# Performance work log

Hardware: AMD Instinct MI355X
Metric: run time of the kernel (lower is better)

Reference implementation:

```python
import jax, jax.numpy as jnp
import numpy as np

ATT = 512  # attention_size

def setup_inputs() -> dict:
    key = jax.random.key(0)
    k0, k1, k2, k3, k4 = jax.random.split(key, 5)
    B, Sq, Sk, Din, Dmem = 32, 1024, 1024, 512, 512
    inputs = jax.random.normal(k0, (B, Sq, Din), dtype=jnp.float32)
    memory = jax.random.normal(k1, (B, Sk, Dmem), dtype=jnp.float32)
    memory_mask = jax.random.randint(k2, (B, Sk), 0, 2).astype(jnp.int32)
    W_input = (jax.random.normal(k3, (Din, ATT), dtype=jnp.float32) * 0.02)
    W_memory = (jax.random.normal(k4, (Dmem, ATT), dtype=jnp.float32) * 0.02)
    return {"inputs": inputs, "memory": memory, "memory_mask": memory_mask,
            "W_input": W_input, "W_memory": W_memory}

def reference(inputs, memory, memory_mask, W_input, W_memory):
    # projections (bias=False) + ReLU; dropout=0 -> identity
    x = jax.nn.relu(jnp.einsum('bqd,da->bqa', inputs, W_input))   # [B,Sq,A]
    m = jax.nn.relu(jnp.einsum('bkd,da->bka', memory, W_memory))  # [B,Sk,A]
    scale = 1.0 / jnp.sqrt(jnp.asarray(ATT, dtype=inputs.dtype))
    logits = jnp.einsum('bqa,bka->bqk', x, m) * scale             # [B,Sq,Sk]
    mask = (memory_mask[:, None, :] != 0)                         # [B,1,Sk] broadcast over Sq
    logits = jnp.where(mask, logits, jnp.asarray(-1e30, dtype=logits.dtype))
    score = jax.nn.softmax(logits, axis=-1)
    context = jnp.einsum('bqk,bkd->bqd', score, memory)           # [B,Sq,Dmem]
    return jnp.concatenate([context, inputs], axis=-1)            # [B,Sq,Dmem+Din]
```

## Files before the change

kernel.cpp:

```cpp
#include <hip/hip_runtime.h>

typedef __bf16 bf16x8 __attribute__((ext_vector_type(8)));
typedef float f32x4 __attribute__((ext_vector_type(4)));

__device__ __forceinline__ unsigned short f2bf(float f) {
    union { float f; unsigned u; } v; v.f = f;
    unsigned r = v.u + 0x7FFFu + ((v.u >> 16) & 1u);
    return (unsigned short)(r >> 16);
}

__global__ __launch_bounds__(256) void prep_kernel(
    const float4* __restrict__ inputs4, uint2* __restrict__ InB16,
    float4* __restrict__ out4,
    const float* __restrict__ W0, const float* __restrict__ W1,
    unsigned short* __restrict__ D0, unsigned short* __restrict__ D1,
    const int* __restrict__ mask,
    int* __restrict__ cnt, int* __restrict__ padded,
    float4* __restrict__ rowsum4,
    const float* __restrict__ memory,
    unsigned short* __restrict__ MemG, unsigned short* __restrict__ MemGT)
{
    __shared__ float tile[32][33];
    __shared__ float tileG[32][132];
    __shared__ int wsum[4];
    __shared__ int kidx32[32];
    const int bid = blockIdx.x;
    const int t = threadIdx.x;

    if (bid < 1024) {
        const int b = bid >> 5;
        const int jt = bid & 31;
        const int j0 = jt * 32;
        const int* m = mask + b * 1024;
        int v[4]; int s = 0;
#pragma unroll
        for (int e = 0; e < 4; e++) { v[e] = (m[t * 4 + e] != 0) ? 1 : 0; s += v[e]; }
        const int lane = t & 63, wv = t >> 6;
        int x = s;
#pragma unroll
        for (int off = 1; off < 64; off <<= 1) {
            int y = __shfl_up(x, off, 64);
            if (lane >= off) x += y;
        }
        if (lane == 63) wsum[wv] = x;
        __syncthreads();
        int base = 0;
        for (int w = 0; w < wv; w++) base += wsum[w];
        const int nb = wsum[0] + wsum[1] + wsum[2] + wsum[3];
        const int pb = (nb + 127) & ~127;
        if (j0 >= pb) return;
        int pos = base + x - s;
#pragma unroll
        for (int e = 0; e < 4; e++)
            if (v[e]) {
                int p = pos++;
                if (p >= j0 && p < j0 + 32) kidx32[p - j0] = t * 4 + e;
            }
        __syncthreads();

        const float4* src4 = (const float4*)(memory + (size_t)b * 1024 * 512);
        const int jj = t >> 3;
        const int cq = t & 7;
        const bool live = (j0 + jj) < nb;
        const int krow = live ? kidx32[jj] : 0;

        float4 vv[4][4];
        if (live) {
            const float4* rp = src4 + (size_t)krow * 128 + cq * 4;
#pragma unroll
            for (int c = 0; c < 4; c++)
#pragma unroll
                for (int i = 0; i < 4; i++) vv[c][i] = rp[c * 32 + i];
        } else {
#pragma unroll
            for (int c = 0; c < 4; c++)
#pragma unroll
                for (int i = 0; i < 4; i++) vv[c][i] = float4{0.f, 0.f, 0.f, 0.f};
        }

        unsigned short* mg = MemG + (size_t)b * 1024 * 512 + (size_t)(j0 + jj) * 512;
#pragma unroll
        for (int c = 0; c < 4; c++) {
            union { unsigned short u[16]; uint4 q[2]; } pk;
#pragma unroll
            for (int i = 0; i < 4; i++) {
                pk.u[i * 4 + 0] = f2bf(vv[c][i].x); pk.u[i * 4 + 1] = f2bf(vv[c][i].y);
                pk.u[i * 4 + 2] = f2bf(vv[c][i].z); pk.u[i * 4 + 3] = f2bf(vv[c][i].w);
            }
            *(uint4*)&mg[c * 128 + cq * 16] = pk.q[0];
            *(uint4*)&mg[c * 128 + cq * 16 + 8] = pk.q[1];
        }

        const int dd = t >> 1;
        const int jh = (t & 1) * 16;
        unsigned short* gtb = MemGT + (size_t)b * 512 * 1024 + j0 + jh;
#pragma unroll
        for (int c = 0; c < 4; c++) {
#pragma unroll
            for (int i = 0; i < 4; i++)
                *(float4*)&tileG[jj][cq * 16 + i * 4] = vv[c][i];
            __syncthreads();
            union { unsigned short u[16]; uint4 q[2]; } pt;
#pragma unroll
            for (int k = 0; k < 16; k++) pt.u[k] = f2bf(tileG[jh + k][dd]);
            unsigned short* gt = gtb + (size_t)(c * 128 + dd) * 1024;
            *(uint4*)&gt[0] = pt.q[0];
            *(uint4*)&gt[8] = pt.q[1];
            __syncthreads();
        }
    } else if (bid < 1056) {
        const int b = bid - 1024;
        rowsum4[b * 256 + t] = float4{0.f, 0.f, 0.f, 0.f};
        const int* m = mask + b * 1024;
        int s = 0;
#pragma unroll
        for (int e = 0; e < 4; e++) s += (m[t * 4 + e] != 0) ? 1 : 0;
        const int lane = t & 63, wv = t >> 6;
        int x = s;
#pragma unroll
        for (int off = 1; off < 64; off <<= 1) {
            int y = __shfl_up(x, off, 64);
            if (lane >= off) x += y;
        }
        if (lane == 63) wsum[wv] = x;
        __syncthreads();
        if (t == 255) {
            int total = wsum[0] + wsum[1] + wsum[2] + wsum[3];
            cnt[b] = total;
            padded[b] = (total + 127) & ~127;
        }
    } else if (bid < 1568) {
        const int tb = bid - 1056;
        const float* src = (tb >> 8) ? W1 : W0;
        unsigned short* dst = (tb >> 8) ? D1 : D0;
        const int rem = tb & 255;
        const int s0 = (rem & 15) * 32, d0 = (rem >> 4) * 32;
        const int tr = t >> 5, tc = t & 31;
#pragma unroll
        for (int i = 0; i < 4; i++)
            tile[tr + i * 8][tc] = src[(size_t)(s0 + tr + i * 8) * 512 + d0 + tc];
        __syncthreads();
#pragma unroll
        for (int i = 0; i < 4; i++)
            dst[(size_t)(d0 + tr + i * 8) * 512 + s0 + tc] = f2bf(tile[tc][tr + i * 8]);
    } else {
        const int i = (bid - 1568) * 256 + t;
        const int bq = i >> 7;
        const int d  = i & 127;
        float4 v = inputs4[i];
        out4[(size_t)bq * 256 + 128 + d] = v;
        union { unsigned short u[4]; uint2 p; } pk;
        pk.u[0] = f2bf(v.x); pk.u[1] = f2bf(v.y);
        pk.u[2] = f2bf(v.z); pk.u[3] = f2bf(v.w);
        InB16[i] = pk.p;
    }
}

template<int CMODE>
__device__ __forceinline__ void gemm_core(
    unsigned char* lds,
    const unsigned short* __restrict__ Ab, const unsigned short* __restrict__ Bb,
    void* __restrict__ Cb, float* __restrict__ rs, int nbv,
    int rowA, int rowB, int Kz, int lda, int ldb, int ldc, float scale)
{
    const int nt = Kz >> 6;

    const int t = threadIdx.x;
    const int w = t >> 6;
    const int lane = t & 63;
    const int wm = w >> 2;
    const int wn = w & 3;
    const int l15 = lane & 15;
    const int sx = (((lane >> 4) ^ ((l15 >> 1) & 3)) << 4);

    const int r0 = t >> 2;
    const int sl = (t & 3) ^ ((t >> 3) & 3);
    const unsigned short* aS0 = Ab + (size_t)(rowA + r0) * lda + sl * 8;
    const unsigned short* aS1 = aS0 + (size_t)128 * lda;
    const unsigned short* bS0 = Bb + (size_t)(rowB + r0) * ldb + sl * 8;
    const unsigned short* bS1 = bS0 + (size_t)128 * ldb;

    const int wofs = w * 1024;
    const int aRd = (wm * 128 + l15) * 64 + sx;
    const int bRd = 32768 + (wn * 64 + l15) * 64 + sx;

    f32x4 acc[8][4];
#pragma unroll
    for (int i = 0; i < 8; i++)
#pragma unroll
        for (int j = 0; j < 4; j++) acc[i][j] = f32x4{0.f, 0.f, 0.f, 0.f};

#define GLL(SRC, DOFS) __builtin_amdgcn_global_load_lds(                        \
        (const __attribute__((address_space(1))) void*)(SRC),                   \
        (__attribute__((address_space(3))) void*)&lds[DOFS], 16, 0, 0)
#define STAGEA(BUF, KH, KEL) do {                                               \
        GLL(aS0 + (KEL), (BUF) * 65536 + (KH) * 16384 + wofs);                  \
        GLL(aS1 + (KEL), (BUF) * 65536 + (KH) * 16384 + wofs + 8192); } while (0)
#define STAGEB(BUF, KH, KEL) do {                                               \
        GLL(bS0 + (KEL), (BUF) * 65536 + 32768 + (KH) * 16384 + wofs);          \
        GLL(bS1 + (KEL), (BUF) * 65536 + 32768 + (KH) * 16384 + wofs + 8192); } while (0)

    STAGEA(0, 0, 0); STAGEB(0, 0, 0); STAGEA(0, 1, 32); STAGEB(0, 1, 32);
    asm volatile("s_waitcnt vmcnt(4)" ::: "memory");
    __builtin_amdgcn_s_barrier();

    for (int tt = 0; tt < nt; ++tt) {
        const int cur = (tt & 1) * 65536;
        const int nxt = (tt & 1) ^ 1;
        const bool pf = (tt + 1) < nt;
        const int kn = (tt + 1) * 64;
        bf16x8 af[4], bf0[4], bf1[4];

#pragma unroll
        for (int i = 0; i < 4; i++) af[i]  = *(const bf16x8*)&lds[cur + aRd + i * 1024];
#pragma unroll
        for (int j = 0; j < 4; j++) bf0[j] = *(const bf16x8*)&lds[cur + bRd + j * 1024];
        if (pf) STAGEA(nxt, 0, kn);
        __builtin_amdgcn_s_barrier();
        asm volatile("s_waitcnt lgkmcnt(0)" ::: "memory");
        __builtin_amdgcn_sched_barrier(0);
        __builtin_amdgcn_s_setprio(1);
#pragma unroll
        for (int i = 0; i < 4; i++)
#pragma unroll
            for (int j = 0; j < 4; j++)
                acc[i][j] = __builtin_amdgcn_mfma_f32_16x16x32_bf16(af[i], bf0[j], acc[i][j], 0, 0, 0);
        __builtin_amdgcn_s_setprio(0);
        __builtin_amdgcn_s_barrier();

#pragma unroll
        for (int i = 0; i < 4; i++) af[i] = *(const bf16x8*)&lds[cur + aRd + (i + 4) * 1024];
        if (pf) STAGEB(nxt, 0, kn);
        __builtin_amdgcn_s_barrier();
        asm volatile("s_waitcnt lgkmcnt(0)" ::: "memory");
        __builtin_amdgcn_sched_barrier(0);
        __builtin_amdgcn_s_setprio(1);
#pragma unroll
        for (int i = 0; i < 4; i++)
#pragma unroll
            for (int j = 0; j < 4; j++)
                acc[i + 4][j] = __builtin_amdgcn_mfma_f32_16x16x32_bf16(af[i], bf0[j], acc[i + 4][j], 0, 0, 0);
        __builtin_amdgcn_s_setprio(0);
        if (pf) { asm volatile("s_waitcnt vmcnt(4)" ::: "memory"); }
        else    { asm volatile("s_waitcnt vmcnt(0)" ::: "memory"); }
        __builtin_amdgcn_s_barrier();

#pragma unroll
        for (int i = 0; i < 4; i++) af[i]  = *(const bf16x8*)&lds[cur + 16384 + aRd + i * 1024];
#pragma unroll
        for (int j = 0; j < 4; j++) bf1[j] = *(const bf16x8*)&lds[cur + 16384 + bRd + j * 1024];
        if (pf) STAGEA(nxt, 1, kn + 32);
        __builtin_amdgcn_s_barrier();
        asm volatile("s_waitcnt lgkmcnt(0)" ::: "memory");
        __builtin_amdgcn_sched_barrier(0);
        __builtin_amdgcn_s_setprio(1);
#pragma unroll
        for (int i = 0; i < 4; i++)
#pragma unroll
            for (int j = 0; j < 4; j++)
                acc[i][j] = __builtin_amdgcn_mfma_f32_16x16x32_bf16(af[i], bf1[j], acc[i][j], 0, 0, 0);
        __builtin_amdgcn_s_setprio(0);
        __builtin_amdgcn_s_barrier();

#pragma unroll
        for (int i = 0; i < 4; i++) af[i] = *(const bf16x8*)&lds[cur + 16384 + aRd + (i + 4) * 1024];
        if (pf) STAGEB(nxt, 1, kn + 32);
        __builtin_amdgcn_s_barrier();
        asm volatile("s_waitcnt lgkmcnt(0)" ::: "memory");
        __builtin_amdgcn_sched_barrier(0);
        __builtin_amdgcn_s_setprio(1);
#pragma unroll
        for (int i = 0; i < 4; i++)
#pragma unroll
            for (int j = 0; j < 4; j++)
                acc[i + 4][j] = __builtin_amdgcn_mfma_f32_16x16x32_bf16(af[i], bf1[j], acc[i + 4][j], 0, 0, 0);
        __builtin_amdgcn_s_setprio(0);
        if (pf) { asm volatile("s_waitcnt vmcnt(4)" ::: "memory"); }
        __builtin_amdgcn_s_barrier();
    }

#undef GLL
#undef STAGEA
#undef STAGEB

    const int orow = (lane >> 4) * 4;
    const int ocol = l15;

    if constexpr (CMODE == 0) {
        unsigned short* C = (unsigned short*)Cb;
#pragma unroll
        for (int mf = 0; mf < 8; mf++)
#pragma unroll
            for (int nf = 0; nf < 4; nf++) {
                const int col = rowB + wn * 64 + nf * 16 + ocol;
#pragma unroll
                for (int r = 0; r < 4; r++) {
                    const int rw = rowA + wm * 128 + mf * 16 + orow + r;
                    C[(size_t)rw * ldc + col] = f2bf(fmaxf(acc[mf][nf][r], 0.f));
                }
            }
    } else if constexpr (CMODE == 1) {
        unsigned short* C = (unsigned short*)Cb;
#pragma unroll
        for (int mf = 0; mf < 8; mf++) {
            float part[4] = {0.f, 0.f, 0.f, 0.f};
#pragma unroll
            for (int nf = 0; nf < 4; nf++) {
                const int col = rowB + wn * 64 + nf * 16 + ocol;
#pragma unroll
                for (int r = 0; r < 4; r++) {
                    float p = (col < nbv) ? __expf(acc[mf][nf][r] * scale) : 0.f;
                    part[r] += p;
                    const int rw = rowA + wm * 128 + mf * 16 + orow + r;
                    C[(size_t)rw * ldc + col] = f2bf(p);
                }
            }
#pragma unroll
            for (int r = 0; r < 4; r++) {
                float s = part[r];
                s += __shfl_xor(s, 1, 64);
                s += __shfl_xor(s, 2, 64);
                s += __shfl_xor(s, 4, 64);
                s += __shfl_xor(s, 8, 64);
                if (ocol == 0)
                    atomicAdd(&rs[rowA + wm * 128 + mf * 16 + orow + r], s);
            }
        }
    } else {
        float* C = (float*)Cb;
#pragma unroll
        for (int mf = 0; mf < 8; mf++) {
            float inv[4];
#pragma unroll
            for (int r = 0; r < 4; r++)
                inv[r] = 1.0f / rs[rowA + wm * 128 + mf * 16 + orow + r];
#pragma unroll
            for (int nf = 0; nf < 4; nf++) {
                const int col = rowB + wn * 64 + nf * 16 + ocol;
#pragma unroll
                for (int r = 0; r < 4; r++) {
                    const int rw = rowA + wm * 128 + mf * 16 + orow + r;
                    C[(size_t)rw * ldc + col] = acc[mf][nf][r] * inv[r];
                }
            }
        }
    }
}

__global__ __launch_bounds__(512, 2) void gemm_proj_kernel(
    const unsigned short* __restrict__ InB16, const unsigned short* __restrict__ WtIn,
    unsigned short* __restrict__ Xq,
    const unsigned short* __restrict__ MemG, const unsigned short* __restrict__ WtMem,
    unsigned short* __restrict__ Xm, const int* __restrict__ padded)
{
    __shared__ __align__(16) unsigned char lds[131072];
    const int id = blockIdx.x;
    const int xcd = id & 7, slot = id >> 3;
    const int y = xcd + 8 * (slot >> 1);
    const int x = slot & 1;
    const int rowB = x * 256;
    const unsigned short* A;
    const unsigned short* Bt;
    unsigned short* C;
    int rowA;
    if (y < 128) {
        A = InB16; Bt = WtIn; C = Xq; rowA = y * 256;
    } else {
        const int idx = y - 128;
        const int z = idx >> 2;
        rowA = (idx & 3) * 256;
        if (rowA >= padded[z]) return;
        A = MemG + (size_t)z * 524288;
        Bt = WtMem;
        C = Xm + (size_t)z * 524288;
    }
    gemm_core<0>(lds, A, Bt, (void*)C, nullptr, 0, rowA, rowB,
                 512, 512, 512, 512, 0.f);
}

__global__ __launch_bounds__(512, 2) void gemm_p_kernel(
    const unsigned short* __restrict__ Xq, const unsigned short* __restrict__ Xm,
    unsigned short* __restrict__ P, const int* __restrict__ cnt,
    const int* __restrict__ padded, float* __restrict__ rowsum, float scale)
{
    __shared__ __align__(16) unsigned char lds[131072];
    const int id = blockIdx.x;
    const int xcd = id & 7, slot = id >> 3;
    const int z = xcd + 8 * (slot >> 4);
    const int r = slot & 15;
    const int x = r & 3, y = r >> 2;
    const int rowB = x * 256;
    if (rowB >= padded[z]) return;
    gemm_core<1>(lds, Xq + (size_t)z * 524288, Xm + (size_t)z * 524288,
                 (void*)(P + (size_t)z * 1048576), rowsum + (size_t)z * 1024, cnt[z],
                 y * 256, rowB, 512, 512, 512, 1024, scale);
}

__global__ __launch_bounds__(512, 2) void gemm_ctx_kernel(
    const unsigned short* __restrict__ P, const unsigned short* __restrict__ MemGT,
    float* __restrict__ out, const int* __restrict__ padded, float* __restrict__ rowsum)
{
    __shared__ __align__(16) unsigned char lds[131072];
    const int id = blockIdx.x;
    const int xcd = id & 7, slot = id >> 3;
    const int z = xcd + 8 * (slot >> 3);
    const int r = slot & 7;
    const int x = r & 1, y = r >> 1;
    gemm_core<2>(lds, P + (size_t)z * 1048576, MemGT + (size_t)z * 524288,
                 (void*)(out + (size_t)z * 1048576), rowsum + (size_t)z * 1024, 0,
                 y * 256, x * 256, padded[z],
                 1024, 1024, 1024, 1.f);
}

extern "C" void kernel_launch(void* const* d_in, const int* in_sizes, int n_in,
                              void* d_out, int out_size, void* d_ws, size_t ws_size,
                              hipStream_t stream)
{
    const float* inputs = (const float*)d_in[0];
    const float* memory = (const float*)d_in[1];
    const int*   mmask  = (const int*)d_in[2];
    const float* W_in   = (const float*)d_in[3];
    const float* W_mem  = (const float*)d_in[4];
    float* out = (float*)d_out;

    char* ws = (char*)d_ws;
    const unsigned long long MB = 1048576ull;
    unsigned short* Wt_in  = (unsigned short*)(ws);
    unsigned short* Wt_mem = (unsigned short*)(ws + 524288);
    unsigned short* InB16  = (unsigned short*)(ws + 1 * MB);
    unsigned short* MemG   = (unsigned short*)(ws + 33 * MB);
    unsigned short* P      = (unsigned short*)(ws + 1 * MB);
    unsigned short* MemGT  = (unsigned short*)(ws + 65 * MB);
    unsigned short* Xq     = (unsigned short*)(ws + 97 * MB);
    unsigned short* Xm     = (unsigned short*)(ws + 129 * MB);
    float*          rowsum = (float*)(ws + 161 * MB);
    int*            cntp   = (int*)(ws + 161 * MB + 262144);
    int*            padp   = (int*)(ws + 161 * MB + 262144 + 128);

    const float scale = 0.04419417382415922f;

    prep_kernel<<<17952, 256, 0, stream>>>(
        (const float4*)inputs, (uint2*)InB16, (float4*)out,
        W_in, W_mem, Wt_in, Wt_mem,
        mmask, cntp, padp, (float4*)rowsum,
        memory, MemG, MemGT);

    gemm_proj_kernel<<<512, 512, 0, stream>>>(
        InB16, Wt_in, Xq, MemG, Wt_mem, Xm, padp);

    gemm_p_kernel<<<512, 512, 0, stream>>>(
        Xq, Xm, P, cntp, padp, rowsum, scale);

    gemm_ctx_kernel<<<256, 512, 0, stream>>>(
        P, MemGT, out, padp, rowsum);
}
```

Before: 363.4 us.

## Shrink GEMM block tiles to 128x128 with 4 waves and more blocks

Changes the shared GEMM core from 256x256 tiles with 8 waves to 128x128 tiles with 4 waves, each wave computing a 64x64 sub-tile. LDS is halved to 64 KB, the k-loop is restructured into two half-steps, and all three GEMM kernels are relaunched with four times as many 256-thread blocks using new XCD-aware index mappings. The aim is better load balance and occupancy, especially where padding-based early exits leave 256-wide tiles idle. In exchange, each block reuses less data, so global and LDS traffic per FLOP goes up.

Result: no change. 366.8 us (+0.9%).

```diff
diff --git a/kernel.cpp b/kernel.cpp
--- a/kernel.cpp
+++ b/kernel.cpp
@@ -168,25 +168,25 @@
     const int t = threadIdx.x;
     const int w = t >> 6;
     const int lane = t & 63;
-    const int wm = w >> 2;
-    const int wn = w & 3;
+    const int wm = w >> 1;
+    const int wn = w & 1;
     const int l15 = lane & 15;
     const int sx = (((lane >> 4) ^ ((l15 >> 1) & 3)) << 4);
 
     const int r0 = t >> 2;
     const int sl = (t & 3) ^ ((t >> 3) & 3);
     const unsigned short* aS0 = Ab + (size_t)(rowA + r0) * lda + sl * 8;
-    const unsigned short* aS1 = aS0 + (size_t)128 * lda;
+    const unsigned short* aS1 = aS0 + (size_t)64 * lda;
     const unsigned short* bS0 = Bb + (size_t)(rowB + r0) * ldb + sl * 8;
-    const unsigned short* bS1 = bS0 + (size_t)128 * ldb;
+    const unsigned short* bS1 = bS0 + (size_t)64 * ldb;
 
     const int wofs = w * 1024;
-    const int aRd = (wm * 128 + l15) * 64 + sx;
-    const int bRd = 32768 + (wn * 64 + l15) * 64 + sx;
-
-    f32x4 acc[8][4];
-#pragma unroll
-    for (int i = 0; i < 8; i++)
+    const int aRd = (wm * 64 + l15) * 64 + sx;
+    const int bRd = 16384 + (wn * 64 + l15) * 64 + sx;
+
+    f32x4 acc[4][4];
+#pragma unroll
+    for (int i = 0; i < 4; i++)
 #pragma unroll
         for (int j = 0; j < 4; j++) acc[i][j] = f32x4{0.f, 0.f, 0.f, 0.f};
 
@@ -194,28 +194,28 @@
         (const __attribute__((address_space(1))) void*)(SRC),                   \
         (__attribute__((address_space(3))) void*)&lds[DOFS], 16, 0, 0)
 #define STAGEA(BUF, KH, KEL) do {                                               \
-        GLL(aS0 + (KEL), (BUF) * 65536 + (KH) * 16384 + wofs);                  \
-        GLL(aS1 + (KEL), (BUF) * 65536 + (KH) * 16384 + wofs + 8192); } while (0)
+        GLL(aS0 + (KEL), (BUF) * 32768 + (KH) * 8192 + wofs);                   \
+        GLL(aS1 + (KEL), (BUF) * 32768 + (KH) * 8192 + wofs + 4096); } while (0)
 #define STAGEB(BUF, KH, KEL) do {                                               \
-        GLL(bS0 + (KEL), (BUF) * 65536 + 32768 + (KH) * 16384 + wofs);          \
-        GLL(bS1 + (KEL), (BUF) * 65536 + 32768 + (KH) * 16384 + wofs + 8192); } while (0)
+        GLL(bS0 + (KEL), (BUF) * 32768 + 16384 + (KH) * 8192 + wofs);           \
+        GLL(bS1 + (KEL), (BUF) * 32768 + 16384 + (KH) * 8192 + wofs + 4096); } while (0)
 
     STAGEA(0, 0, 0); STAGEB(0, 0, 0); STAGEA(0, 1, 32); STAGEB(0, 1, 32);
     asm volatile("s_waitcnt vmcnt(4)" ::: "memory");
     __builtin_amdgcn_s_barrier();
 
     for (int tt = 0; tt < nt; ++tt) {
-        const int cur = (tt & 1) * 65536;
+        const int cur = (tt & 1) * 32768;
         const int nxt = (tt & 1) ^ 1;
         const bool pf = (tt + 1) < nt;
         const int kn = (tt + 1) * 64;
-        bf16x8 af[4], bf0[4], bf1[4];
+        bf16x8 af[4], bfr[4];
 
 #pragma unroll
         for (int i = 0; i < 4; i++) af[i]  = *(const bf16x8*)&lds[cur + aRd + i * 1024];
 #pragma unroll
-        for (int j = 0; j < 4; j++) bf0[j] = *(const bf16x8*)&lds[cur + bRd + j * 1024];
-        if (pf) STAGEA(nxt, 0, kn);
+        for (int j = 0; j < 4; j++) bfr[j] = *(const bf16x8*)&lds[cur + bRd + j * 1024];
+        if (pf) { STAGEA(nxt, 0, kn); STAGEB(nxt, 0, kn); }
         __builtin_amdgcn_s_barrier();
         asm volatile("s_waitcnt lgkmcnt(0)" ::: "memory");
         __builtin_amdgcn_sched_barrier(0);
@@ -224,13 +224,17 @@
         for (int i = 0; i < 4; i++)
 #pragma unroll
             for (int j = 0; j < 4; j++)
-                acc[i][j] = __builtin_amdgcn_mfma_f32_16x16x32_bf16(af[i], bf0[j], acc[i][j], 0, 0, 0);
+                acc[i][j] = __builtin_amdgcn_mfma_f32_16x16x32_bf16(af[i], bfr[j], acc[i][j], 0, 0, 0);
         __builtin_amdgcn_s_setprio(0);
+        if (pf) { asm volatile("s_waitcnt vmcnt(4)" ::: "memory"); }
+        else    { asm volatile("s_waitcnt vmcnt(0)" ::: "memory"); }
         __builtin_amdgcn_s_barrier();
 
 #pragma unroll
-        for (int i = 0; i < 4; i++) af[i] = *(const bf16x8*)&lds[cur + aRd + (i + 4) * 1024];
-        if (pf) STAGEB(nxt, 0, kn);
+        for (int i = 0; i < 4; i++) af[i]  = *(const bf16x8*)&lds[cur + 8192 + aRd + i * 1024];
+#pragma unroll
+        for (int j = 0; j < 4; j++) bfr[j] = *(const bf16x8*)&lds[cur + 8192 + bRd + j * 1024];
+        if (pf) { STAGEA(nxt, 1, kn + 32); STAGEB(nxt, 1, kn + 32); }
         __builtin_amdgcn_s_barrier();
         asm volatile("s_waitcnt lgkmcnt(0)" ::: "memory");
         __builtin_amdgcn_sched_barrier(0);
@@ -239,41 +243,7 @@
         for (int i = 0; i < 4; i++)
 #pragma unroll
             for (int j = 0; j < 4; j++)
-                acc[i + 4][j] = __builtin_amdgcn_mfma_f32_16x16x32_bf16(af[i], bf0[j], acc[i + 4][j], 0, 0, 0);
-        __builtin_amdgcn_s_setprio(0);
-        if (pf) { asm volatile("s_waitcnt vmcnt(4)" ::: "memory"); }
-        else    { asm volatile("s_waitcnt vmcnt(0)" ::: "memory"); }
-        __builtin_amdgcn_s_barrier();
-
-#pragma unroll
-        for (int i = 0; i < 4; i++) af[i]  = *(const bf16x8*)&lds[cur + 16384 + aRd + i * 1024];
-#pragma unroll
-        for (int j = 0; j < 4; j++) bf1[j] = *(const bf16x8*)&lds[cur + 16384 + bRd + j * 1024];
-        if (pf) STAGEA(nxt, 1, kn + 32);
-        __builtin_amdgcn_s_barrier();
-        asm volatile("s_waitcnt lgkmcnt(0)" ::: "memory");
-        __builtin_amdgcn_sched_barrier(0);
-        __builtin_amdgcn_s_setprio(1);
-#pragma unroll
-        for (int i = 0; i < 4; i++)
-#pragma unroll
-            for (int j = 0; j < 4; j++)
-                acc[i][j] = __builtin_amdgcn_mfma_f32_16x16x32_bf16(af[i], bf1[j], acc[i][j], 0, 0, 0);
-        __builtin_amdgcn_s_setprio(0);
-        __builtin_amdgcn_s_barrier();
-
-#pragma unroll
-        for (int i = 0; i < 4; i++) af[i] = *(const bf16x8*)&lds[cur + 16384 + aRd + (i + 4) * 1024];
-        if (pf) STAGEB(nxt, 1, kn + 32);
-        __builtin_amdgcn_s_barrier();
-        asm volatile("s_waitcnt lgkmcnt(0)" ::: "memory");
-        __builtin_amdgcn_sched_barrier(0);
-        __builtin_amdgcn_s_setprio(1);
-#pragma unroll
-        for (int i = 0; i < 4; i++)
-#pragma unroll
-            for (int j = 0; j < 4; j++)
-                acc[i + 4][j] = __builtin_amdgcn_mfma_f32_16x16x32_bf16(af[i], bf1[j], acc[i + 4][j], 0, 0, 0);
+                acc[i][j] = __builtin_amdgcn_mfma_f32_16x16x32_bf16(af[i], bfr[j], acc[i][j], 0, 0, 0);
         __builtin_amdgcn_s_setprio(0);
         if (pf) { asm volatile("s_waitcnt vmcnt(4)" ::: "memory"); }
         __builtin_amdgcn_s_barrier();
@@ -289,20 +259,20 @@
     if constexpr (CMODE == 0) {
         unsigned short* C = (unsigned short*)Cb;
 #pragma unroll
-        for (int mf = 0; mf < 8; mf++)
+        for (int mf = 0; mf < 4; mf++)
 #pragma unroll
             for (int nf = 0; nf < 4; nf++) {
                 const int col = rowB + wn * 64 + nf * 16 + ocol;
 #pragma unroll
                 for (int r = 0; r < 4; r++) {
-                    const int rw = rowA + wm * 128 + mf * 16 + orow + r;
+                    const int rw = rowA + wm * 64 + mf * 16 + orow + r;
                     C[(size_t)rw * ldc + col] = f2bf(fmaxf(acc[mf][nf][r], 0.f));
                 }
             }
     } else if constexpr (CMODE == 1) {
         unsigned short* C = (unsigned short*)Cb;
 #pragma unroll
-        for (int mf = 0; mf < 8; mf++) {
+        for (int mf = 0; mf < 4; mf++) {
             float part[4] = {0.f, 0.f, 0.f, 0.f};
 #pragma unroll
             for (int nf = 0; nf < 4; nf++) {
@@ -311,7 +281,7 @@
                 for (int r = 0; r < 4; r++) {
                     float p = (col < nbv) ? __expf(acc[mf][nf][r] * scale) : 0.f;
                     part[r] += p;
-                    const int rw = rowA + wm * 128 + mf * 16 + orow + r;
+                    const int rw = rowA + wm * 64 + mf * 16 + orow + r;
                     C[(size_t)rw * ldc + col] = f2bf(p);
                 }
             }
@@ -323,23 +293,23 @@
                 s += __shfl_xor(s, 4, 64);
                 s += __shfl_xor(s, 8, 64);
                 if (ocol == 0)
-                    atomicAdd(&rs[rowA + wm * 128 + mf * 16 + orow + r], s);
+                    atomicAdd(&rs[rowA + wm * 64 + mf * 16 + orow + r], s);
             }
         }
     } else {
         float* C = (float*)Cb;
 #pragma unroll
-        for (int mf = 0; mf < 8; mf++) {
+        for (int mf = 0; mf < 4; mf++) {
             float inv[4];
 #pragma unroll
             for (int r = 0; r < 4; r++)
-                inv[r] = 1.0f / rs[rowA + wm * 128 + mf * 16 + orow + r];
+                inv[r] = 1.0f / rs[rowA + wm * 64 + mf * 16 + orow + r];
 #pragma unroll
             for (int nf = 0; nf < 4; nf++) {
                 const int col = rowB + wn * 64 + nf * 16 + ocol;
 #pragma unroll
                 for (int r = 0; r < 4; r++) {
-                    const int rw = rowA + wm * 128 + mf * 16 + orow + r;
+                    const int rw = rowA + wm * 64 + mf * 16 + orow + r;
                     C[(size_t)rw * ldc + col] = acc[mf][nf][r] * inv[r];
                 }
             }
@@ -347,28 +317,28 @@
     }
 }
 
-__global__ __launch_bounds__(512, 2) void gemm_proj_kernel(
+__global__ __launch_bounds__(256, 2) void gemm_proj_kernel(
     const unsigned short* __restrict__ InB16, const unsigned short* __restrict__ WtIn,
     unsigned short* __restrict__ Xq,
     const unsigned short* __restrict__ MemG, const unsigned short* __restrict__ WtMem,
     unsigned short* __restrict__ Xm, const int* __restrict__ padded)
 {
-    __shared__ __align__(16) unsigned char lds[131072];
+    __shared__ __align__(16) unsigned char lds[65536];
     const int id = blockIdx.x;
-    const int xcd = id & 7, slot = id >> 3;
-    const int y = xcd + 8 * (slot >> 1);
-    const int x = slot & 1;
-    const int rowB = x * 256;
+    const int xcd = id & 7, u8 = id >> 3;
+    const int y = xcd + 8 * (u8 >> 2);
+    const int x = u8 & 3;
+    const int rowB = x * 128;
     const unsigned short* A;
     const unsigned short* Bt;
     unsigned short* C;
     int rowA;
-    if (y < 128) {
-        A = InB16; Bt = WtIn; C = Xq; rowA = y * 256;
+    if (y < 256) {
+        A = InB16; Bt = WtIn; C = Xq; rowA = y * 128;
     } else {
-        const int idx = y - 128;
-        const int z = idx >> 2;
-        rowA = (idx & 3) * 256;
+        const int idx = y - 256;
+        const int z = idx >> 3;
+        rowA = (idx & 7) * 128;
         if (rowA >= padded[z]) return;
         A = MemG + (size_t)z * 524288;
         Bt = WtMem;
@@ -378,37 +348,37 @@
                  512, 512, 512, 512, 0.f);
 }
 
-__global__ __launch_bounds__(512, 2) void gemm_p_kernel(
+__global__ __launch_bounds__(256, 2) void gemm_p_kernel(
     const unsigned short* __restrict__ Xq, const unsigned short* __restrict__ Xm,
     unsigned short* __restrict__ P, const int* __restrict__ cnt,
     const int* __restrict__ padded, float* __restrict__ rowsum, float scale)
 {
-    __shared__ __align__(16) unsigned char lds[131072];
+    __shared__ __align__(16) unsigned char lds[65536];
     const int id = blockIdx.x;
-    const int xcd = id & 7, slot = id >> 3;
-    const int z = xcd + 8 * (slot >> 4);
-    const int r = slot & 15;
-    const int x = r & 3, y = r >> 2;
-    const int rowB = x * 256;
+    const int xcd = id & 7, u = id >> 3;
+    const int z = xcd + 8 * (u >> 6);
+    const int r = u & 63;
+    const int x = r & 7, y = r >> 3;
+    const int rowB = x * 128;
     if (rowB >= padded[z]) return;
     gemm_core<1>(lds, Xq + (size_t)z * 524288, Xm + (size_t)z * 524288,
                  (void*)(P + (size_t)z * 1048576), rowsum + (size_t)z * 1024, cnt[z],
-                 y * 256, rowB, 512, 512, 512, 1024, scale);
-}
-
-__global__ __launch_bounds__(512, 2) void gemm_ctx_kernel(
+                 y * 128, rowB, 512, 512, 512, 1024, scale);
+}
+
+__global__ __launch_bounds__(256, 2) void gemm_ctx_kernel(
     const unsigned short* __restrict__ P, const unsigned short* __restrict__ MemGT,
     float* __restrict__ out, const int* __restrict__ padded, float* __restrict__ rowsum)
 {
-    __shared__ __align__(16) unsigned char lds[131072];
+    __shared__ __align__(16) unsigned char lds[65536];
     const int id = blockIdx.x;
-    const int xcd = id & 7, slot = id >> 3;
-    const int z = xcd + 8 * (slot >> 3);
-    const int r = slot & 7;
-    const int x = r & 1, y = r >> 1;
+    const int xcd = id & 7, u = id >> 3;
+    const int z = xcd + 8 * (u >> 5);
+    const int r = u & 31;
+    const int x = r & 3, y = r >> 2;
     gemm_core<2>(lds, P + (size_t)z * 1048576, MemGT + (size_t)z * 524288,
                  (void*)(out + (size_t)z * 1048576), rowsum + (size_t)z * 1024, 0,
-                 y * 256, x * 256, padded[z],
+                 y * 128, x * 128, padded[z],
                  1024, 1024, 1024, 1.f);
 }
 
@@ -445,12 +415,12 @@
         mmask, cntp, padp, (float4*)rowsum,
         memory, MemG, MemGT);
 
-    gemm_proj_kernel<<<512, 512, 0, stream>>>(
+    gemm_proj_kernel<<<2048, 256, 0, stream>>>(
         InB16, Wt_in, Xq, MemG, Wt_mem, Xm, padp);
 
-    gemm_p_kernel<<<512, 512, 0, stream>>>(
+    gemm_p_kernel<<<2048, 256, 0, stream>>>(
         Xq, Xm, P, cntp, padp, rowsum, scale);
 
-    gemm_ctx_kernel<<<256, 512, 0, stream>>>(
+    gemm_ctx_kernel<<<1024, 256, 0, stream>>>(
         P, MemGT, out, padp, rowsum);
 }
```
